# Performance work log

Hardware: AMD Instinct MI355X
Metric: run time of the kernel (lower is better)

## Reference

```python
import jax, jax.numpy as jnp
import numpy as np

N_HEADS = 32
N_KV_HEADS = 8
HEAD_DIM = 128  # hidden 4096 / 32
NEG_INF = -1e9


def _apply_rope(x, cos, sin):
    # x: [B, S, H, D]; cos/sin: [S, D//2] -> complex multiply on (even, odd) pairs
    B, S, H, D = x.shape
    xr = x.reshape(B, S, H, D // 2, 2)
    a, b = xr[..., 0], xr[..., 1]
    c = cos[None, :, None, :]
    s = sin[None, :, None, :]
    out = jnp.stack([a * c - b * s, a * s + b * c], axis=-1)
    return out.reshape(B, S, H, D)


def setup_inputs() -> dict:
    key = jax.random.key(0)
    ks = jax.random.split(key, 8)
    B, S, HID = 1, 2048, 4096
    hidden_states = jax.random.normal(ks[0], (B, S, HID), dtype=jnp.float32)
    # causal additive mask [1,1,S,S]
    causal = jnp.tril(jnp.ones((S, S), dtype=bool))
    attention_mask = jnp.where(causal, 0.0, NEG_INF).astype(jnp.float32)[None, None]
    # true rotary frequencies (theta=500000 as in llama3)
    half = HEAD_DIM // 2
    inv_freq = 1.0 / (500000.0 ** (np.arange(0, half, dtype=np.float32) / half))
    angles = np.arange(S, dtype=np.float32)[:, None] * inv_freq[None, :]
    freqs_cos = jnp.asarray(np.cos(angles), dtype=jnp.float32)
    freqs_sin = jnp.asarray(np.sin(angles), dtype=jnp.float32)
    sc = 0.02
    wq = jax.random.normal(ks[1], (HID, HID), dtype=jnp.float32) * sc
    wk = jax.random.normal(ks[2], (N_KV_HEADS * HEAD_DIM, HID), dtype=jnp.float32) * sc
    wv = jax.random.normal(ks[3], (N_KV_HEADS * HEAD_DIM, HID), dtype=jnp.float32) * sc
    wo = jax.random.normal(ks[4], (HID, HID), dtype=jnp.float32) * sc
    return {"hidden_states": hidden_states, "attention_mask": attention_mask,
            "freqs_cos": freqs_cos, "freqs_sin": freqs_sin,
            "wq": wq, "wk": wk, "wv": wv, "wo": wo}


def reference(hidden_states, attention_mask, freqs_cos, freqs_sin, wq, wk, wv, wo):
    B, S, HID = hidden_states.shape
    n_rep = N_HEADS // N_KV_HEADS
    # projections (torch Linear: x @ W.T)
    q = (hidden_states @ wq.T).reshape(B, S, N_HEADS, HEAD_DIM)
    k = (hidden_states @ wk.T).reshape(B, S, N_KV_HEADS, HEAD_DIM)
    v = (hidden_states @ wv.T).reshape(B, S, N_KV_HEADS, HEAD_DIM)
    # rotary on q (full cos/sin) and k
    q = _apply_rope(q, freqs_cos, freqs_sin)
    k = _apply_rope(k, freqs_cos, freqs_sin)
    # [B, H, S, D]
    q = q.transpose(0, 2, 1, 3)
    k = k.transpose(0, 2, 1, 3)
    v = v.transpose(0, 2, 1, 3)
    # GQA: repeat_interleave kv heads
    k = jnp.repeat(k, n_rep, axis=1)
    v = jnp.repeat(v, n_rep, axis=1)
    scores = jnp.einsum("bhqd,bhkd->bhqk", q, k) / jnp.sqrt(jnp.float32(HEAD_DIM))
    scores = scores + attention_mask
    probs = jax.nn.softmax(scores.astype(jnp.float32), axis=-1)
    attn = jnp.einsum("bhqk,bhkd->bhqd", probs, v)
    attn = attn.transpose(0, 2, 1, 3).reshape(B, S, N_HEADS * HEAD_DIM)
    return attn @ wo.T
```

## Files before the change

kernel.cpp:

```cpp
#include <hip/hip_runtime.h>
#include <hip/hip_bf16.h>
#include <math.h>

#define SEQ 2048
#define HID 4096
#define NH 32
#define NKV 8
#define HD 128
#define KVG (NH / NKV)
#define NQKV 6144

typedef __bf16 bf16x8 __attribute__((ext_vector_type(8)));
typedef float  f32x4  __attribute__((ext_vector_type(4)));

__device__ __forceinline__ unsigned short f2bf(float f) {
  union { float f; unsigned int u; } v; v.f = f;
  unsigned int r = v.u + 0x7FFFu + ((v.u >> 16) & 1u);
  return (unsigned short)(r >> 16);
}
__device__ __forceinline__ float bf2f(unsigned short h) {
  union { unsigned int u; float f; } v; v.u = ((unsigned int)h) << 16;
  return v.f;
}

__device__ __forceinline__ void glds16(const unsigned short* g, unsigned short* l) {
  __builtin_amdgcn_global_load_lds(
      (const __attribute__((address_space(1))) void*)g,
      (__attribute__((address_space(3))) void*)l, 16, 0, 0);
}

__global__ __launch_bounds__(256) void cvt_all(
    const float* __restrict__ H, const float* __restrict__ wq,
    const float* __restrict__ wk, const float* __restrict__ wv,
    const float* __restrict__ wo, unsigned short* __restrict__ ws)
{
  const long G1 = 1l << 20;
  const long M1 = 1l << 20;
  long g = (long)blockIdx.x * 256 + threadIdx.x;
  const float* src; unsigned short* dst; long rel;
  if      (g < 2 * G1) { src = H;  dst = ws;           rel = g;          }
  else if (g < 6 * G1) { src = wq; dst = ws + 8 * M1;  rel = g - 2 * G1; }
  else if (g < 7 * G1) { src = wk; dst = ws + 24 * M1; rel = g - 6 * G1; }
  else if (g < 8 * G1) { src = wv; dst = ws + 28 * M1; rel = g - 7 * G1; }
  else                 { src = wo; dst = ws + 32 * M1; rel = g - 8 * G1; }
  float4 v = ((const float4*)src)[rel];
  ushort4 o;
  o.x = f2bf(v.x); o.y = f2bf(v.y); o.z = f2bf(v.z); o.w = f2bf(v.w);
  ((ushort4*)dst)[rel] = o;
}

template<bool F32OUT>
__global__ __launch_bounds__(256) void gemm_nt(
    const unsigned short* __restrict__ A,
    const unsigned short* __restrict__ B,
    void* __restrict__ Cv,
    int M, int N, int K)
{
  __shared__ unsigned short As[128 * 64];
  __shared__ unsigned short Bs[128 * 64];
  const int t = threadIdx.x;
  const int lane = t & 63, wid = t >> 6;
  const int quad = lane >> 4, l16 = lane & 15;
  const int wm = (wid & 1) * 64, wn = (wid >> 1) * 64;
  const int m0 = blockIdx.y * 128, n0 = blockIdx.x * 128;

  int srow[4], sgch[4];
  const unsigned short* ga[4];
  const unsigned short* gb[4];
  unsigned short* la[4];
  unsigned short* lb[4];
  #pragma unroll
  for (int j = 0; j < 4; j++) {
    int pj = (wid * 4 + j) * 64 + lane;
    srow[j] = pj >> 3;
    sgch[j] = (pj & 7) ^ (srow[j] & 7);
    ga[j] = A + (size_t)(m0 + srow[j]) * K + sgch[j] * 8;
    gb[j] = B + (size_t)(n0 + srow[j]) * K + sgch[j] * 8;
    la[j] = &As[(wid * 4 + j) * 512];
    lb[j] = &Bs[(wid * 4 + j) * 512];
  }

  const f32x4 fzero = {0.f, 0.f, 0.f, 0.f};
  f32x4 acc[4][4];
  #pragma unroll
  for (int i = 0; i < 4; i++)
    #pragma unroll
    for (int j = 0; j < 4; j++) acc[i][j] = fzero;

  for (int k0 = 0; k0 < K; k0 += 64) {
    __syncthreads();
    #pragma unroll
    for (int j = 0; j < 4; j++) {
      glds16(ga[j], la[j]);
      glds16(gb[j], lb[j]);
      ga[j] += 64; gb[j] += 64;
    }
    __syncthreads();

    #pragma unroll
    for (int ks = 0; ks < 2; ks++) {
      bf16x8 af[4], bfr[4];
      #pragma unroll
      for (int mt = 0; mt < 4; mt++) {
        int row = wm + mt * 16 + l16;
        int cp = (ks * 4 + quad) ^ (l16 & 7);
        af[mt] = *(const bf16x8*)(&As[(row * 8 + cp) * 8]);
      }
      #pragma unroll
      for (int nt = 0; nt < 4; nt++) {
        int row = wn + nt * 16 + l16;
        int cp = (ks * 4 + quad) ^ (l16 & 7);
        bfr[nt] = *(const bf16x8*)(&Bs[(row * 8 + cp) * 8]);
      }
      #pragma unroll
      for (int mt = 0; mt < 4; mt++)
        #pragma unroll
        for (int nt = 0; nt < 4; nt++)
          acc[mt][nt] = __builtin_amdgcn_mfma_f32_16x16x32_bf16(af[mt], bfr[nt], acc[mt][nt], 0, 0, 0);
    }
  }

  #pragma unroll
  for (int mt = 0; mt < 4; mt++)
    #pragma unroll
    for (int nt = 0; nt < 4; nt++)
      #pragma unroll
      for (int r = 0; r < 4; r++) {
        int row = m0 + wm + mt * 16 + quad * 4 + r;
        int col = n0 + wn + nt * 16 + l16;
        float v = acc[mt][nt][r];
        if (F32OUT) ((float*)Cv)[(size_t)row * N + col] = v;
        else        ((unsigned short*)Cv)[(size_t)row * N + col] = f2bf(v);
      }
}

__global__ __launch_bounds__(256) void rope_vtrans(
    const unsigned short* __restrict__ QKVr,
    const float* __restrict__ cosT,
    const float* __restrict__ sinT,
    unsigned short* __restrict__ Qh,
    unsigned short* __restrict__ Kh,
    unsigned short* __restrict__ Vtg)
{
  __shared__ unsigned short T[64 * 66];
  int hh = blockIdx.y;
  int bx = blockIdx.x;
  int t = threadIdx.x;
  if (hh < NH + NKV) {
    int sub = t >> 6, d2 = t & 63;
    int s = bx * 4 + sub;
    float c = cosT[s * 64 + d2], sn = sinT[s * 64 + d2];
    if (hh < NH) {
      const unsigned short* src = QKVr + (size_t)s * NQKV + hh * HD;
      unsigned short* dst = Qh + ((size_t)hh * SEQ + s) * HD;
      float a = bf2f(src[2 * d2]), b = bf2f(src[2 * d2 + 1]);
      dst[2 * d2]     = f2bf(a * c - b * sn);
      dst[2 * d2 + 1] = f2bf(a * sn + b * c);
    } else {
      int h = hh - NH;
      const unsigned short* src = QKVr + (size_t)s * NQKV + HID + h * HD;
      unsigned short* dst = Kh + ((size_t)h * SEQ + s) * HD;
      float a = bf2f(src[2 * d2]), b = bf2f(src[2 * d2 + 1]);
      dst[2 * d2]     = f2bf(a * c - b * sn);
      dst[2 * d2 + 1] = f2bf(a * sn + b * c);
    }
  } else {
    int idx = bx >> 5;
    int kvh = idx >> 1, d0 = (idx & 1) * 64;
    int s0 = (bx & 31) * 64;
    int si = t >> 2, dchunk = t & 3;
    const unsigned short* src = QKVr + (size_t)(s0 + si) * NQKV + HID + NKV * HD + kvh * HD + d0 + dchunk * 16;
    uint4 a = *(const uint4*)src;
    uint4 b = *(const uint4*)(src + 8);
    unsigned int va[8] = {a.x, a.y, a.z, a.w, b.x, b.y, b.z, b.w};
    #pragma unroll
    for (int j = 0; j < 8; j++)
      *(unsigned int*)(&T[si * 66 + dchunk * 16 + j * 2]) = va[j];
    __syncthreads();
    int di = t >> 2, schunk = t & 3;
    unsigned short px[16];
    #pragma unroll
    for (int j = 0; j < 16; j++) px[j] = T[(schunk * 16 + j) * 66 + di];
    unsigned short* dst = Vtg + ((size_t)kvh * HD + d0 + di) * SEQ + s0 + schunk * 16;
    *(uint4*)dst = *(uint4*)px;
    *(uint4*)(dst + 8) = *(uint4*)(px + 8);
  }
}

__global__ __launch_bounds__(256) void flash_kernel(
    const unsigned short* __restrict__ Qh,
    const unsigned short* __restrict__ Kh,
    const unsigned short* __restrict__ Vtg,
    unsigned short* __restrict__ Obf)
{
  __shared__ unsigned short Ks[64 * 128];
  __shared__ unsigned short Vs[128 * 64];
  __shared__ unsigned short Ps[4][16 * 72];

  const int h = blockIdx.y;
  const int pairp = blockIdx.x;
  const int kvh = h / KVG;
  const int t = threadIdx.x;
  const int lane = t & 63, w = t >> 6;
  const int quad = lane >> 4, l16 = lane & 15;
  const float scale = 0.08838834764831845f;
  const float SHIFT = 8.0f;

  bf16x8 ones;
  #pragma unroll
  for (int j = 0; j < 8; j++) ones[j] = (__bf16)1.0f;

  int krow[4], kgch[4], vrow[4], vgch[4];
  unsigned short* lk[4];
  unsigned short* lv[4];
  #pragma unroll
  for (int j = 0; j < 4; j++) {
    int pj = (w * 4 + j) * 64 + lane;
    krow[j] = pj >> 4; kgch[j] = (pj & 15) ^ (krow[j] & 15);
    vrow[j] = pj >> 3; vgch[j] = (pj & 7) ^ (vrow[j] & 7);
    lk[j] = &Ks[(w * 4 + j) * 512];
    lv[j] = &Vs[(w * 4 + j) * 512];
  }

  unsigned short* Pw = Ps[w];
  const f32x4 fzero = {0.f, 0.f, 0.f, 0.f};

  #pragma unroll
  for (int pass = 0; pass < 2; pass++) {
    const int qt = pass ? (31 - pairp) : pairp;
    const int q0 = qt * 64;
    const int q = q0 + w * 16 + l16;

    bf16x8 aq[4];
    const unsigned short* Qp = Qh + ((size_t)h * SEQ + q0 + w * 16 + l16) * HD;
    #pragma unroll
    for (int ks = 0; ks < 4; ks++) aq[ks] = *(const bf16x8*)(Qp + ks * 32 + quad * 8);

    f32x4 o[8];
    #pragma unroll
    for (int dt = 0; dt < 8; dt++) o[dt] = fzero;
    f32x4 lacc = fzero;

    const unsigned short* gk[4];
    const unsigned short* gv[4];
    #pragma unroll
    for (int j = 0; j < 4; j++) {
      gk[j] = Kh + ((size_t)kvh * SEQ + krow[j]) * HD + kgch[j] * 8;
      gv[j] = Vtg + ((size_t)kvh * HD + vrow[j]) * SEQ + vgch[j] * 8;
    }

    for (int kv0 = 0; kv0 <= q0; kv0 += 64) {
      __syncthreads();
      #pragma unroll
      for (int j = 0; j < 4; j++) {
        glds16(gk[j], lk[j]);
        glds16(gv[j], lv[j]);
        gk[j] += 64 * HD;
        gv[j] += 64;
      }
      __syncthreads();

      f32x4 sc[4];
      #pragma unroll
      for (int kvt = 0; kvt < 4; kvt++) sc[kvt] = fzero;
      #pragma unroll
      for (int ks = 0; ks < 4; ks++)
        #pragma unroll
        for (int kvt = 0; kvt < 4; kvt++) {
          int row = kvt * 16 + l16;
          int cp = (ks * 4 + quad) ^ l16;
          bf16x8 bk = *(const bf16x8*)(&Ks[(row * 16 + cp) * 8]);
          sc[kvt] = __builtin_amdgcn_mfma_f32_16x16x32_bf16(bk, aq[ks], sc[kvt], 0, 0, 0);
        }

      #pragma unroll
      for (int kvt = 0; kvt < 4; kvt++) {
        unsigned short ph[4];
        #pragma unroll
        for (int r = 0; r < 4; r++) {
          int kv = kv0 + kvt * 16 + quad * 4 + r;
          float p = (kv > q) ? 0.f : __expf(fmaf(sc[kvt][r], scale, -SHIFT));
          ph[r] = f2bf(p);
        }
        *(uint2*)(&Pw[l16 * 72 + kvt * 16 + quad * 4]) = *(const uint2*)ph;
      }

      #pragma unroll
      for (int ks2 = 0; ks2 < 2; ks2++) {
        bf16x8 ap = *(const bf16x8*)(&Pw[l16 * 72 + ks2 * 32 + quad * 8]);
        lacc = __builtin_amdgcn_mfma_f32_16x16x32_bf16(ap, ones, lacc, 0, 0, 0);
        #pragma unroll
        for (int dt = 0; dt < 8; dt++) {
          int row = dt * 16 + l16;
          int cp = (ks2 * 4 + quad) ^ (l16 & 7);
          bf16x8 bv = *(const bf16x8*)(&Vs[(row * 8 + cp) * 8]);
          o[dt] = __builtin_amdgcn_mfma_f32_16x16x32_bf16(ap, bv, o[dt], 0, 0, 0);
        }
      }
    }

    #pragma unroll
    for (int dt = 0; dt < 8; dt++)
      #pragma unroll
      for (int r = 0; r < 4; r++) {
        int qq = q0 + w * 16 + quad * 4 + r;
        int d = dt * 16 + l16;
        Obf[(size_t)qq * HID + h * HD + d] = f2bf(o[dt][r] / lacc[r]);
      }
  }
}

extern "C" void kernel_launch(void* const* d_in, const int* in_sizes, int n_in,
                              void* d_out, int out_size, void* d_ws, size_t ws_size,
                              hipStream_t stream) {
  const float* H    = (const float*)d_in[0];
  const float* cosT = (const float*)d_in[2];
  const float* sinT = (const float*)d_in[3];
  const float* wq   = (const float*)d_in[4];
  const float* wk   = (const float*)d_in[5];
  const float* wv   = (const float*)d_in[6];
  const float* wo   = (const float*)d_in[7];

  unsigned short* ws = (unsigned short*)d_ws;
  const size_t M1 = 1u << 20;
  unsigned short* Hb   = ws;
  unsigned short* Wqkv = ws + (size_t)8  * M1;
  unsigned short* Wob  = ws + (size_t)32 * M1;
  unsigned short* QKVr = ws + (size_t)48 * M1;
  unsigned short* Qh   = ws + (size_t)8  * M1;
  unsigned short* Kh   = ws + (size_t)16 * M1;
  unsigned short* Vtg  = ws + (size_t)18 * M1;
  unsigned short* attn = ws;

  cvt_all<<<49152, 256, 0, stream>>>(H, wq, wk, wv, wo, ws);

  gemm_nt<false><<<dim3(48, 16), 256, 0, stream>>>(Hb, Wqkv, QKVr, SEQ, NQKV, HID);

  rope_vtrans<<<dim3(512, NH + NKV + 1), 256, 0, stream>>>(QKVr, cosT, sinT, Qh, Kh, Vtg);

  flash_kernel<<<dim3(16, NH), 256, 0, stream>>>(Qh, Kh, Vtg, attn);

  gemm_nt<true><<<dim3(32, 16), 256, 0, stream>>>(attn, Wob, d_out, SEQ, HID, HID);
}
```

Measured before the change: 478.5 us.

## Double flash-attention query tile per block and vectorize RoPE loads/stores

```diff
diff --git a/kernel.cpp b/kernel.cpp
--- a/kernel.cpp
+++ b/kernel.cpp
@@ -150,20 +150,20 @@
     int sub = t >> 6, d2 = t & 63;
     int s = bx * 4 + sub;
     float c = cosT[s * 64 + d2], sn = sinT[s * 64 + d2];
+    const unsigned short* src;
+    unsigned short* dst;
     if (hh < NH) {
-      const unsigned short* src = QKVr + (size_t)s * NQKV + hh * HD;
-      unsigned short* dst = Qh + ((size_t)hh * SEQ + s) * HD;
-      float a = bf2f(src[2 * d2]), b = bf2f(src[2 * d2 + 1]);
-      dst[2 * d2]     = f2bf(a * c - b * sn);
-      dst[2 * d2 + 1] = f2bf(a * sn + b * c);
+      src = QKVr + (size_t)s * NQKV + hh * HD;
+      dst = Qh + ((size_t)hh * SEQ + s) * HD;
     } else {
       int h = hh - NH;
-      const unsigned short* src = QKVr + (size_t)s * NQKV + HID + h * HD;
-      unsigned short* dst = Kh + ((size_t)h * SEQ + s) * HD;
-      float a = bf2f(src[2 * d2]), b = bf2f(src[2 * d2 + 1]);
-      dst[2 * d2]     = f2bf(a * c - b * sn);
-      dst[2 * d2 + 1] = f2bf(a * sn + b * c);
-    }
+      src = QKVr + (size_t)s * NQKV + HID + h * HD;
+      dst = Kh + ((size_t)h * SEQ + s) * HD;
+    }
+    unsigned int u = *(const unsigned int*)(src + 2 * d2);
+    float a = bf2f((unsigned short)(u & 0xffff)), b = bf2f((unsigned short)(u >> 16));
+    unsigned int o = (unsigned int)f2bf(a * c - b * sn) | ((unsigned int)f2bf(a * sn + b * c) << 16);
+    *(unsigned int*)(dst + 2 * d2) = o;
   } else {
     int idx = bx >> 5;
     int kvh = idx >> 1, d0 = (idx & 1) * 64;
@@ -195,7 +195,7 @@
 {
   __shared__ unsigned short Ks[64 * 128];
   __shared__ unsigned short Vs[128 * 64];
-  __shared__ unsigned short Ps[4][16 * 72];
+  __shared__ unsigned short Ps[4][32 * 72];
 
   const int h = blockIdx.y;
   const int pairp = blockIdx.x;
@@ -227,19 +227,24 @@
 
   #pragma unroll
   for (int pass = 0; pass < 2; pass++) {
-    const int qt = pass ? (31 - pairp) : pairp;
-    const int q0 = qt * 64;
-    const int q = q0 + w * 16 + l16;
-
-    bf16x8 aq[4];
-    const unsigned short* Qp = Qh + ((size_t)h * SEQ + q0 + w * 16 + l16) * HD;
-    #pragma unroll
-    for (int ks = 0; ks < 4; ks++) aq[ks] = *(const bf16x8*)(Qp + ks * 32 + quad * 8);
-
-    f32x4 o[8];
-    #pragma unroll
-    for (int dt = 0; dt < 8; dt++) o[dt] = fzero;
-    f32x4 lacc = fzero;
+    const int qt = pass ? (15 - pairp) : pairp;
+    const int q0 = qt * 128;
+    const int qw = q0 + w * 32;
+
+    bf16x8 aq[2][4];
+    #pragma unroll
+    for (int qg = 0; qg < 2; qg++) {
+      const unsigned short* Qp = Qh + ((size_t)h * SEQ + qw + qg * 16 + l16) * HD;
+      #pragma unroll
+      for (int ks = 0; ks < 4; ks++) aq[qg][ks] = *(const bf16x8*)(Qp + ks * 32 + quad * 8);
+    }
+
+    f32x4 o[2][8];
+    #pragma unroll
+    for (int qg = 0; qg < 2; qg++)
+      #pragma unroll
+      for (int dt = 0; dt < 8; dt++) o[qg][dt] = fzero;
+    f32x4 lacc[2] = {fzero, fzero};
 
     const unsigned short* gk[4];
     const unsigned short* gv[4];
@@ -249,7 +254,7 @@
       gv[j] = Vtg + ((size_t)kvh * HD + vrow[j]) * SEQ + vgch[j] * 8;
     }
 
-    for (int kv0 = 0; kv0 <= q0; kv0 += 64) {
+    for (int kv0 = 0; kv0 < q0 + 128; kv0 += 64) {
       __syncthreads();
       #pragma unroll
       for (int j = 0; j < 4; j++) {
@@ -260,9 +265,11 @@
       }
       __syncthreads();
 
-      f32x4 sc[4];
-      #pragma unroll
-      for (int kvt = 0; kvt < 4; kvt++) sc[kvt] = fzero;
+      f32x4 sc[2][4];
+      #pragma unroll
+      for (int qg = 0; qg < 2; qg++)
+        #pragma unroll
+        for (int kvt = 0; kvt < 4; kvt++) sc[qg][kvt] = fzero;
       #pragma unroll
       for (int ks = 0; ks < 4; ks++)
         #pragma unroll
@@ -270,43 +277,53 @@
           int row = kvt * 16 + l16;
           int cp = (ks * 4 + quad) ^ l16;
           bf16x8 bk = *(const bf16x8*)(&Ks[(row * 16 + cp) * 8]);
-          sc[kvt] = __builtin_amdgcn_mfma_f32_16x16x32_bf16(bk, aq[ks], sc[kvt], 0, 0, 0);
+          sc[0][kvt] = __builtin_amdgcn_mfma_f32_16x16x32_bf16(bk, aq[0][ks], sc[0][kvt], 0, 0, 0);
+          sc[1][kvt] = __builtin_amdgcn_mfma_f32_16x16x32_bf16(bk, aq[1][ks], sc[1][kvt], 0, 0, 0);
         }
 
       #pragma unroll
-      for (int kvt = 0; kvt < 4; kvt++) {
-        unsigned short ph[4];
-        #pragma unroll
-        for (int r = 0; r < 4; r++) {
-          int kv = kv0 + kvt * 16 + quad * 4 + r;
-          float p = (kv > q) ? 0.f : __expf(fmaf(sc[kvt][r], scale, -SHIFT));
-          ph[r] = f2bf(p);
+      for (int qg = 0; qg < 2; qg++) {
+        int q = qw + qg * 16 + l16;
+        #pragma unroll
+        for (int kvt = 0; kvt < 4; kvt++) {
+          unsigned short ph[4];
+          #pragma unroll
+          for (int r = 0; r < 4; r++) {
+            int kv = kv0 + kvt * 16 + quad * 4 + r;
+            float p = (kv > q) ? 0.f : __expf(fmaf(sc[qg][kvt][r], scale, -SHIFT));
+            ph[r] = f2bf(p);
+          }
+          *(uint2*)(&Pw[(qg * 16 + l16) * 72 + kvt * 16 + quad * 4]) = *(const uint2*)ph;
         }
-        *(uint2*)(&Pw[l16 * 72 + kvt * 16 + quad * 4]) = *(const uint2*)ph;
       }
 
       #pragma unroll
       for (int ks2 = 0; ks2 < 2; ks2++) {
-        bf16x8 ap = *(const bf16x8*)(&Pw[l16 * 72 + ks2 * 32 + quad * 8]);
-        lacc = __builtin_amdgcn_mfma_f32_16x16x32_bf16(ap, ones, lacc, 0, 0, 0);
+        bf16x8 ap0 = *(const bf16x8*)(&Pw[(l16)      * 72 + ks2 * 32 + quad * 8]);
+        bf16x8 ap1 = *(const bf16x8*)(&Pw[(16 + l16) * 72 + ks2 * 32 + quad * 8]);
+        lacc[0] = __builtin_amdgcn_mfma_f32_16x16x32_bf16(ap0, ones, lacc[0], 0, 0, 0);
+        lacc[1] = __builtin_amdgcn_mfma_f32_16x16x32_bf16(ap1, ones, lacc[1], 0, 0, 0);
         #pragma unroll
         for (int dt = 0; dt < 8; dt++) {
           int row = dt * 16 + l16;
           int cp = (ks2 * 4 + quad) ^ (l16 & 7);
           bf16x8 bv = *(const bf16x8*)(&Vs[(row * 8 + cp) * 8]);
-          o[dt] = __builtin_amdgcn_mfma_f32_16x16x32_bf16(ap, bv, o[dt], 0, 0, 0);
+          o[0][dt] = __builtin_amdgcn_mfma_f32_16x16x32_bf16(ap0, bv, o[0][dt], 0, 0, 0);
+          o[1][dt] = __builtin_amdgcn_mfma_f32_16x16x32_bf16(ap1, bv, o[1][dt], 0, 0, 0);
         }
       }
     }
 
     #pragma unroll
-    for (int dt = 0; dt < 8; dt++)
-      #pragma unroll
-      for (int r = 0; r < 4; r++) {
-        int qq = q0 + w * 16 + quad * 4 + r;
-        int d = dt * 16 + l16;
-        Obf[(size_t)qq * HID + h * HD + d] = f2bf(o[dt][r] / lacc[r]);
-      }
+    for (int qg = 0; qg < 2; qg++)
+      #pragma unroll
+      for (int dt = 0; dt < 8; dt++)
+        #pragma unroll
+        for (int r = 0; r < 4; r++) {
+          int qq = qw + qg * 16 + quad * 4 + r;
+          int d = dt * 16 + l16;
+          Obf[(size_t)qq * HID + h * HD + d] = f2bf(o[qg][dt][r] / lacc[qg][r]);
+        }
   }
 }
 
@@ -338,7 +355,7 @@
 
   rope_vtrans<<<dim3(512, NH + NKV + 1), 256, 0, stream>>>(QKVr, cosT, sinT, Qh, Kh, Vtg);
 
-  flash_kernel<<<dim3(16, NH), 256, 0, stream>>>(Qh, Kh, Vtg, attn);
+  flash_kernel<<<dim3(8, NH), 256, 0, stream>>>(Qh, Kh, Vtg, attn);
 
   gemm_nt<true><<<dim3(32, 16), 256, 0, stream>>>(attn, Wob, d_out, SEQ, HID, HID);
 }
```

After: 490.4 us. +2.5%, slower.
